# Kernel tuning notes

Measured on AMD Instinct MI355X. Metric: run time of the kernel, lower is better.

## Reference

```python
import jax, jax.numpy as jnp
import numpy as np

EPS = 1e-5

def _bn_train(h, gamma, beta):
    # BatchNorm1d in training mode: batch mean and biased variance over batch dim
    mu = jnp.mean(h, axis=0)
    var = jnp.mean((h - mu) ** 2, axis=0)
    return (h - mu) * jax.lax.rsqrt(var + EPS) * gamma + beta

def setup_inputs() -> dict:
    key = jax.random.key(0)
    ks = jax.random.split(key, 12)
    B, IN, H1, H2, NC = 16384, 4096, 256, 128, 12
    x = jax.random.normal(ks[0], (B, 1, 64, 64), dtype=jnp.float32)
    y = jax.random.randint(ks[1], (B,), 0, NC, dtype=jnp.int32)
    s1 = 1.0 / np.sqrt(IN)
    W1 = jax.random.uniform(ks[2], (H1, IN), jnp.float32, -s1, s1)
    b1 = jax.random.uniform(ks[3], (H1,), jnp.float32, -s1, s1)
    g1 = jax.random.normal(ks[4], (H1,), jnp.float32) * 0.1 + 1.0
    be1 = jax.random.normal(ks[5], (H1,), jnp.float32) * 0.1
    s2 = 1.0 / np.sqrt(H1)
    W2 = jax.random.uniform(ks[6], (H2, H1), jnp.float32, -s2, s2)
    b2 = jax.random.uniform(ks[7], (H2,), jnp.float32, -s2, s2)
    g2 = jax.random.normal(ks[8], (H2,), jnp.float32) * 0.1 + 1.0
    be2 = jax.random.normal(ks[9], (H2,), jnp.float32) * 0.1
    s4 = 1.0 / np.sqrt(H2)
    W4 = jax.random.uniform(ks[10], (NC, H2), jnp.float32, -s4, s4)
    b4 = jax.random.uniform(ks[11], (NC,), jnp.float32, -s4, s4)
    return {"x": x, "W1": W1, "b1": b1, "g1": g1, "be1": be1,
            "W2": W2, "b2": b2, "g2": g2, "be2": be2,
            "W4": W4, "b4": b4, "y": y}

def reference(x, W1, b1, g1, be1, W2, b2, g2, be2, W4, b4, y):
    B = x.shape[0]
    h = x.reshape(B, -1)  # [B, 4096]
    # layer 1: binarized linear + BN(train) + hardtanh (dropout p=0 is identity)
    h = h @ jnp.sign(W1).T + jnp.sign(b1)
    h = jnp.clip(_bn_train(h, g1, be1), -1.0, 1.0)
    # layer 2
    h = h @ jnp.sign(W2).T + jnp.sign(b2)
    h = jnp.clip(_bn_train(h, g2, be2), -1.0, 1.0)
    # final float linear
    return h @ W4.T + b4  # [B, 12]
```

## Files before the change

kernel.cpp:

```cpp
#include <hip/hip_runtime.h>
#include <cstddef>

typedef __attribute__((ext_vector_type(8))) short short8;
typedef __attribute__((ext_vector_type(4))) float f4;
typedef __attribute__((ext_vector_type(4))) unsigned int u4;

__device__ __forceinline__ unsigned int f2bf(float f){
  unsigned int u = __float_as_uint(f);
  u += 0x7fffu + ((u >> 16) & 1u);
  return u >> 16;
}
__device__ __forceinline__ float bflo(unsigned int w){ return __uint_as_float((w & 0xFFFFu) << 16); }
__device__ __forceinline__ float bfhi(unsigned int w){ return __uint_as_float(w & 0xFFFF0000u); }
__device__ __forceinline__ float fsign(float x){ return (x > 0.f) ? 1.f : ((x < 0.f) ? -1.f : 0.f); }
__device__ __forceinline__ float hclip(float x){ return fminf(1.f, fmaxf(-1.f, x)); }

#define BARRIER() do { \
    __builtin_amdgcn_sched_barrier(0); \
    asm volatile("s_waitcnt lgkmcnt(0)" ::: "memory"); \
    __builtin_amdgcn_s_barrier(); \
    asm volatile("" ::: "memory"); \
    __builtin_amdgcn_sched_barrier(0); \
  } while(0)

__global__ void prep_sign_k(const float* __restrict__ W1, unsigned short* __restrict__ w1s,
                            const float* __restrict__ W2, unsigned short* __restrict__ w2s){
  int i = (blockIdx.x * blockDim.x + threadIdx.x) * 8;
  const float* w; unsigned short* o; int off;
  if (i < 1048576){ w = W1; o = w1s; off = i; }
  else            { w = W2; o = w2s; off = i - 1048576; if (off >= 32768) return; }
  f4 a = *(const f4*)(w + off);
  f4 b = *(const f4*)(w + off + 4);
  unsigned short s[8];
  #pragma unroll
  for (int j = 0; j < 4; j++) s[j]   = (a[j] > 0.f) ? 0x3F80u : ((a[j] < 0.f) ? 0xBF80u : 0u);
  #pragma unroll
  for (int j = 0; j < 4; j++) s[4+j] = (b[j] > 0.f) ? 0x3F80u : ((b[j] < 0.f) ? 0xBF80u : 0u);
  u4 v;
  v.x = (unsigned)s[0] | ((unsigned)s[1] << 16);
  v.y = (unsigned)s[2] | ((unsigned)s[3] << 16);
  v.z = (unsigned)s[4] | ((unsigned)s[5] << 16);
  v.w = (unsigned)s[6] | ((unsigned)s[7] << 16);
  *(u4*)(o + off) = v;
}

__global__ __launch_bounds__(512) void gemm1_k(
    const float* __restrict__ x, const unsigned short* __restrict__ w1s,
    const float* __restrict__ b1, unsigned short* __restrict__ h1,
    float* __restrict__ part1s, float* __restrict__ part1q)
{
  __shared__ __align__(16) char lds[65536];
  const int tid  = threadIdx.x;
  const int lane = tid & 63;
  const int wid  = tid >> 6;
  const int cl   = lane & 15;
  const int g    = lane >> 4;
  const int klo  = g * 8;
  const int row0 = blockIdx.x * 64;

  const int am  = tid >> 3;
  const int ak0 = (tid & 7) * 8;
  const float* xA = x + (size_t)(row0 + am) * 4096 + ak0;
  const int aoff  = ((am * 128) + (ak0 * 2)) ^ ((am & 7) << 4);

  const unsigned short* wbase = w1s + (size_t)(wid * 32 + cl) * 4096 + klo;

  f4 acc[4][2];
  const f4 z = {0.f, 0.f, 0.f, 0.f};
  #pragma unroll
  for (int i = 0; i < 4; i++){ acc[i][0] = z; acc[i][1] = z; }

  f4 rA0a, rA0b, rA1a, rA1b, rA2a, rA2b, rA3a, rA3b;
  short8 Bq0, Bq1, Bq2, Bq3, Br0, Br1, Br2, Br3;

#define LOADA4(KB0) do { \
    rA0a = *(const f4*)(xA + (KB0+0)*64); rA0b = *(const f4*)(xA + (KB0+0)*64 + 4); \
    rA1a = *(const f4*)(xA + (KB0+1)*64); rA1b = *(const f4*)(xA + (KB0+1)*64 + 4); \
    rA2a = *(const f4*)(xA + (KB0+2)*64); rA2b = *(const f4*)(xA + (KB0+2)*64 + 4); \
    rA3a = *(const f4*)(xA + (KB0+3)*64); rA3b = *(const f4*)(xA + (KB0+3)*64 + 4); \
  } while(0)

#define PACK1(DST, RA, RB) do { \
    u4 _v; \
    _v.x = f2bf(RA[0]) | (f2bf(RA[1]) << 16); \
    _v.y = f2bf(RA[2]) | (f2bf(RA[3]) << 16); \
    _v.z = f2bf(RB[0]) | (f2bf(RB[1]) << 16); \
    _v.w = f2bf(RB[2]) | (f2bf(RB[3]) << 16); \
    *(u4*)(DST) = _v; \
  } while(0)

#define WRITEA4(WB) do { \
    PACK1((WB) +     0 + aoff, rA0a, rA0b); \
    PACK1((WB) +  8192 + aoff, rA1a, rA1b); \
    PACK1((WB) + 16384 + aoff, rA2a, rA2b); \
    PACK1((WB) + 24576 + aoff, rA3a, rA3b); \
  } while(0)

#define LOADB(P, KB) do { \
    B##P##0 = *(const short8*)(wbase + (KB)*64); \
    B##P##1 = *(const short8*)(wbase + (KB)*64 + 32); \
    B##P##2 = *(const short8*)(wbase + 65536 + (KB)*64); \
    B##P##3 = *(const short8*)(wbase + 65536 + (KB)*64 + 32); \
  } while(0)

#define COMPUTE(BASE, P) do { \
    const char* _ab = (const char*)(BASE); \
    short8 _af[4][2]; \
    _Pragma("unroll") \
    for (int fm = 0; fm < 4; fm++){ \
      int _m = fm*16 + cl; \
      _af[fm][0] = *(const short8*)(_ab + ((_m*128 + klo*2) ^ ((_m & 7) << 4))); \
      _af[fm][1] = *(const short8*)(_ab + ((_m*128 + (32 + klo)*2) ^ ((_m & 7) << 4))); \
    } \
    _Pragma("unroll") \
    for (int fm = 0; fm < 4; fm++){ \
      acc[fm][0] = __builtin_amdgcn_mfma_f32_16x16x32_bf16(_af[fm][0], B##P##0, acc[fm][0], 0, 0, 0); \
      acc[fm][1] = __builtin_amdgcn_mfma_f32_16x16x32_bf16(_af[fm][0], B##P##2, acc[fm][1], 0, 0, 0); \
      acc[fm][0] = __builtin_amdgcn_mfma_f32_16x16x32_bf16(_af[fm][1], B##P##1, acc[fm][0], 0, 0, 0); \
      acc[fm][1] = __builtin_amdgcn_mfma_f32_16x16x32_bf16(_af[fm][1], B##P##3, acc[fm][1], 0, 0, 0); \
    } \
  } while(0)

  LOADA4(0);
  WRITEA4(lds);
  LOADB(q, 0);
  BARRIER();

  for (int p = 0; p < 16; ++p){
    const bool pg = (p < 15);
    char* rbuf = lds + ((p & 1) << 15);
    char* wbuf = lds + (((p & 1) ^ 1) << 15);
    if (pg) LOADA4(4*p + 4);
    __builtin_amdgcn_sched_barrier(0);
    LOADB(r, 4*p + 1);
    COMPUTE(rbuf,         q);
    LOADB(q, 4*p + 2);
    COMPUTE(rbuf +  8192, r);
    LOADB(r, 4*p + 3);
    COMPUTE(rbuf + 16384, q);
    if (pg) LOADB(q, 4*p + 4);
    COMPUTE(rbuf + 24576, r);
    __builtin_amdgcn_sched_barrier(0);
    if (pg) WRITEA4(wbuf);
    BARRIER();
  }
#undef COMPUTE
#undef LOADB
#undef WRITEA4
#undef PACK1
#undef LOADA4

  #pragma unroll
  for (int fn = 0; fn < 2; fn++){
    int c = wid*32 + fn*16 + cl;
    float sb = fsign(b1[c]);
    float s = 0.f, q = 0.f;
    #pragma unroll
    for (int fm = 0; fm < 4; fm++){
      int rbase = row0 + fm*16 + g*4;
      #pragma unroll
      for (int i = 0; i < 4; i++){
        float v = acc[fm][fn][i] + sb;
        h1[(size_t)(rbase + i)*256 + c] = (unsigned short)f2bf(v);
        s += v; q += v*v;
      }
    }
    s += __shfl_xor(s, 16, 64); s += __shfl_xor(s, 32, 64);
    q += __shfl_xor(q, 16, 64); q += __shfl_xor(q, 32, 64);
    if (g == 0){
      part1s[c*256 + blockIdx.x] = s;
      part1q[c*256 + blockIdx.x] = q;
    }
  }
}

template<int COLS>
__global__ __launch_bounds__(64) void params_k(
    const float* __restrict__ ps, const float* __restrict__ pq,
    const float* __restrict__ g, const float* __restrict__ be,
    float* __restrict__ ab){
  int j = blockIdx.x * 64 + threadIdx.x;
  const f4* vs = (const f4*)(ps + j*256);
  const f4* vq = (const f4*)(pq + j*256);
  f4 s4 = {0,0,0,0}, q4 = {0,0,0,0};
  #pragma unroll 8
  for (int b = 0; b < 64; b++){ s4 += vs[b]; q4 += vq[b]; }
  float s = s4[0]+s4[1]+s4[2]+s4[3];
  float q = q4[0]+q4[1]+q4[2]+q4[3];
  float mu  = s * (1.f/16384.f);
  float var = q * (1.f/16384.f) - mu*mu;
  float a   = g[j] * rsqrtf(var + 1e-5f);
  ab[j] = a;
  ab[COLS + j] = be[j] - mu*a;
}

__global__ __launch_bounds__(512) void gemm2_k(
    const unsigned short* __restrict__ h1, const unsigned short* __restrict__ w2s,
    const float* __restrict__ b2, const float* __restrict__ ab1,
    unsigned short* __restrict__ h2, float* __restrict__ part2s, float* __restrict__ part2q)
{
  __shared__ __align__(16) char lds[32768];
  const int tid  = threadIdx.x;
  const int lane = tid & 63;
  const int wid  = tid >> 6;
  const int cl   = lane & 15;
  const int g    = lane >> 4;
  const int klo  = g * 8;
  const int row0 = blockIdx.x * 64;

  const int am  = tid >> 3;
  const int ak0 = (tid & 7) * 8;
  const unsigned short* hA = h1 + (size_t)(row0 + am) * 256 + ak0;
  const int aw = ((am * 128) + (ak0 * 2)) ^ ((am & 7) << 4);
  const unsigned short* wbase = w2s + (size_t)(wid * 16 + cl) * 256 + klo;

  u4 q0 = *(const u4*)(hA);
  u4 q1 = *(const u4*)(hA + 64);
  u4 q2 = *(const u4*)(hA + 128);
  u4 q3 = *(const u4*)(hA + 192);
  short8 Bq0, Bq1, Br0, Br1;
  Bq0 = *(const short8*)(wbase);
  Bq1 = *(const short8*)(wbase + 32);

#define TRW(KB, RAW) do { \
    f4 _a0 = *(const f4*)(ab1 + (KB)*64 + ak0); \
    f4 _a1 = *(const f4*)(ab1 + (KB)*64 + ak0 + 4); \
    f4 _c0 = *(const f4*)(ab1 + 256 + (KB)*64 + ak0); \
    f4 _c1 = *(const f4*)(ab1 + 256 + (KB)*64 + ak0 + 4); \
    float _t0 = hclip(_a0[0]*bflo(RAW.x) + _c0[0]); \
    float _t1 = hclip(_a0[1]*bfhi(RAW.x) + _c0[1]); \
    float _t2 = hclip(_a0[2]*bflo(RAW.y) + _c0[2]); \
    float _t3 = hclip(_a0[3]*bfhi(RAW.y) + _c0[3]); \
    float _t4 = hclip(_a1[0]*bflo(RAW.z) + _c1[0]); \
    float _t5 = hclip(_a1[1]*bfhi(RAW.z) + _c1[1]); \
    float _t6 = hclip(_a1[2]*bflo(RAW.w) + _c1[2]); \
    float _t7 = hclip(_a1[3]*bfhi(RAW.w) + _c1[3]); \
    u4 _v; \
    _v.x = f2bf(_t0) | (f2bf(_t1) << 16); \
    _v.y = f2bf(_t2) | (f2bf(_t3) << 16); \
    _v.z = f2bf(_t4) | (f2bf(_t5) << 16); \
    _v.w = f2bf(_t6) | (f2bf(_t7) << 16); \
    *(u4*)(lds + (KB)*8192 + aw) = _v; \
  } while(0)

  TRW(0, q0); TRW(1, q1); TRW(2, q2); TRW(3, q3);
#undef TRW
  BARRIER();

  f4 acc[4];
  const f4 z = {0.f, 0.f, 0.f, 0.f};
  #pragma unroll
  for (int i = 0; i < 4; i++) acc[i] = z;

#define LOADB2(P, KB) do { \
    B##P##0 = *(const short8*)(wbase + (KB)*64); \
    B##P##1 = *(const short8*)(wbase + (KB)*64 + 32); \
  } while(0)

#define COMP2(BASE, P) do { \
    const char* _ab = (const char*)(BASE); \
    short8 _af[4][2]; \
    _Pragma("unroll") \
    for (int fm = 0; fm < 4; fm++){ \
      int _m = fm*16 + cl; \
      _af[fm][0] = *(const short8*)(_ab + ((_m*128 + klo*2) ^ ((_m & 7) << 4))); \
      _af[fm][1] = *(const short8*)(_ab + ((_m*128 + (32 + klo)*2) ^ ((_m & 7) << 4))); \
    } \
    _Pragma("unroll") \
    for (int fm = 0; fm < 4; fm++){ \
      acc[fm] = __builtin_amdgcn_mfma_f32_16x16x32_bf16(_af[fm][0], B##P##0, acc[fm], 0, 0, 0); \
      acc[fm] = __builtin_amdgcn_mfma_f32_16x16x32_bf16(_af[fm][1], B##P##1, acc[fm], 0, 0, 0); \
    } \
  } while(0)

  LOADB2(r, 1);
  COMP2(lds,         q);
  LOADB2(q, 2);
  COMP2(lds +  8192, r);
  LOADB2(r, 3);
  COMP2(lds + 16384, q);
  COMP2(lds + 24576, r);
#undef COMP2
#undef LOADB2

  {
    int c = wid*16 + cl;
    float sb = fsign(b2[c]);
    float s = 0.f, q = 0.f;
    #pragma unroll
    for (int fm = 0; fm < 4; fm++){
      int rbase = row0 + fm*16 + g*4;
      #pragma unroll
      for (int i = 0; i < 4; i++){
        float v = acc[fm][i] + sb;
        h2[(size_t)(rbase + i)*128 + c] = (unsigned short)f2bf(v);
        s += v; q += v*v;
      }
    }
    s += __shfl_xor(s, 16, 64); s += __shfl_xor(s, 32, 64);
    q += __shfl_xor(q, 16, 64); q += __shfl_xor(q, 32, 64);
    if (g == 0){
      part2s[c*256 + blockIdx.x] = s;
      part2q[c*256 + blockIdx.x] = q;
    }
  }
}

__global__ __launch_bounds__(64) void final_k(
    const unsigned short* __restrict__ h2, const float* __restrict__ ab2,
    const float* __restrict__ W4, const float* __restrict__ b4,
    float* __restrict__ out)
{
  __shared__ __align__(16) float W4l[12*128];
  __shared__ __align__(16) float a2l[128];
  __shared__ __align__(16) float c2l[128];
  const int t = threadIdx.x;
  #pragma unroll
  for (int i = 0; i < 6; i++)
    *(f4*)&W4l[(i*64 + t)*4] = *(const f4*)(W4 + (i*64 + t)*4);
  a2l[t]      = ab2[t];
  a2l[t + 64] = ab2[t + 64];
  c2l[t]      = ab2[128 + t];
  c2l[t + 64] = ab2[192 + t];
  __syncthreads();

  const int r = blockIdx.x * 64 + t;
  const u4* hp = (const u4*)(h2 + (size_t)r * 128);
  u4 hv0 = hp[0], hv1 = hp[1], hv2 = hp[2],  hv3 = hp[3];
  u4 hv4 = hp[4], hv5 = hp[5], hv6 = hp[6],  hv7 = hp[7];
  u4 hv8 = hp[8], hv9 = hp[9], hv10 = hp[10], hv11 = hp[11];
  u4 hv12 = hp[12], hv13 = hp[13], hv14 = hp[14], hv15 = hp[15];

  float acc[12];
  #pragma unroll
  for (int o = 0; o < 12; o++) acc[o] = b4[o];

#define FPROC(HV, J) do { \
    f4 a0 = *(const f4*)&a2l[(J)*8];     f4 a1 = *(const f4*)&a2l[(J)*8 + 4]; \
    f4 c0 = *(const f4*)&c2l[(J)*8];     f4 c1 = *(const f4*)&c2l[(J)*8 + 4]; \
    float tt0 = hclip(a0[0]*bflo(HV.x) + c0[0]); \
    float tt1 = hclip(a0[1]*bfhi(HV.x) + c0[1]); \
    float tt2 = hclip(a0[2]*bflo(HV.y) + c0[2]); \
    float tt3 = hclip(a0[3]*bfhi(HV.y) + c0[3]); \
    float tt4 = hclip(a1[0]*bflo(HV.z) + c1[0]); \
    float tt5 = hclip(a1[1]*bfhi(HV.z) + c1[1]); \
    float tt6 = hclip(a1[2]*bflo(HV.w) + c1[2]); \
    float tt7 = hclip(a1[3]*bfhi(HV.w) + c1[3]); \
    _Pragma("unroll") \
    for (int o = 0; o < 12; o++){ \
      f4 w0 = *(const f4*)&W4l[o*128 + (J)*8]; \
      f4 w1 = *(const f4*)&W4l[o*128 + (J)*8 + 4]; \
      acc[o] += tt0*w0[0] + tt1*w0[1] + tt2*w0[2] + tt3*w0[3] \
              + tt4*w1[0] + tt5*w1[1] + tt6*w1[2] + tt7*w1[3]; \
    } \
  } while(0)

  FPROC(hv0, 0);  FPROC(hv1, 1);  FPROC(hv2, 2);   FPROC(hv3, 3);
  FPROC(hv4, 4);  FPROC(hv5, 5);  FPROC(hv6, 6);   FPROC(hv7, 7);
  FPROC(hv8, 8);  FPROC(hv9, 9);  FPROC(hv10, 10); FPROC(hv11, 11);
  FPROC(hv12, 12); FPROC(hv13, 13); FPROC(hv14, 14); FPROC(hv15, 15);
#undef FPROC

  #pragma unroll
  for (int o = 0; o < 12; o++) out[(size_t)r*12 + o] = acc[o];
}

extern "C" void kernel_launch(void* const* d_in, const int* in_sizes, int n_in,
                              void* d_out, int out_size, void* d_ws, size_t ws_size,
                              hipStream_t stream)
{
  const float* x   = (const float*)d_in[0];
  const float* W1  = (const float*)d_in[1];
  const float* b1  = (const float*)d_in[2];
  const float* g1  = (const float*)d_in[3];
  const float* be1 = (const float*)d_in[4];
  const float* W2  = (const float*)d_in[5];
  const float* b2  = (const float*)d_in[6];
  const float* g2  = (const float*)d_in[7];
  const float* be2 = (const float*)d_in[8];
  const float* W4  = (const float*)d_in[9];
  const float* b4  = (const float*)d_in[10];
  float* out = (float*)d_out;

  char* ws = (char*)d_ws;
  unsigned short* h1     = (unsigned short*)(ws);
  unsigned short* h2     = (unsigned short*)(ws + 8388608);
  unsigned short* w1s    = (unsigned short*)(ws + 12582912);
  unsigned short* w2s    = (unsigned short*)(ws + 14680064);
  float*          part1s = (float*)(ws + 14745600);
  float*          part1q = (float*)(ws + 15007744);
  float*          part2s = (float*)(ws + 15269888);
  float*          part2q = (float*)(ws + 15400960);
  float*          ab1    = (float*)(ws + 15532032);
  float*          ab2    = (float*)(ws + 15534080);

  prep_sign_k<<<528, 256, 0, stream>>>(W1, w1s, W2, w2s);
  gemm1_k<<<256, 512, 0, stream>>>(x, w1s, b1, h1, part1s, part1q);
  params_k<256><<<4, 64, 0, stream>>>(part1s, part1q, g1, be1, ab1);
  gemm2_k<<<256, 512, 0, stream>>>(h1, w2s, b2, ab1, h2, part2s, part2q);
  params_k<128><<<2, 64, 0, stream>>>(part2s, part2q, g2, be2, ab2);
  final_k<<<256, 64, 0, stream>>>(h2, ab2, W4, b4, out);
}
```

Baseline: 125.5 us.

## Retile gemm1 to 32-row blocks and fold BN param kernels into consumers

gemm1 now uses 256-thread blocks over 32 rows with 4 waves each covering 64 output columns. B fragments for two k-steps are loaded directly from global each iteration, and LDS use drops to 16KB. This doubles the grid to 512 blocks for better occupancy and CU coverage. The two params_k launches are removed: gemm2 reduces the layer-1 partials in every block, and final_k (now 128 threads) reduces the layer-2 partials. This saves launches at the cost of redundant per-block reductions.

```diff
diff --git a/kernel.cpp b/kernel.cpp
--- a/kernel.cpp
+++ b/kernel.cpp
@@ -44,40 +44,52 @@
   *(u4*)(o + off) = v;
 }
 
-__global__ __launch_bounds__(512) void gemm1_k(
+__global__ __launch_bounds__(256, 2) void gemm1_k(
     const float* __restrict__ x, const unsigned short* __restrict__ w1s,
     const float* __restrict__ b1, unsigned short* __restrict__ h1,
     float* __restrict__ part1s, float* __restrict__ part1q)
 {
-  __shared__ __align__(16) char lds[65536];
+  __shared__ __align__(16) char lds[16384];
   const int tid  = threadIdx.x;
   const int lane = tid & 63;
   const int wid  = tid >> 6;
   const int cl   = lane & 15;
   const int g    = lane >> 4;
   const int klo  = g * 8;
-  const int row0 = blockIdx.x * 64;
+  const int row0 = blockIdx.x * 32;
 
   const int am  = tid >> 3;
   const int ak0 = (tid & 7) * 8;
   const float* xA = x + (size_t)(row0 + am) * 4096 + ak0;
   const int aoff  = ((am * 128) + (ak0 * 2)) ^ ((am & 7) << 4);
 
-  const unsigned short* wbase = w1s + (size_t)(wid * 32 + cl) * 4096 + klo;
-
-  f4 acc[4][2];
+  const unsigned short* wbase = w1s + (size_t)(wid * 64 + cl) * 4096 + klo;
+
+  f4 acc[2][4];
   const f4 z = {0.f, 0.f, 0.f, 0.f};
   #pragma unroll
-  for (int i = 0; i < 4; i++){ acc[i][0] = z; acc[i][1] = z; }
-
-  f4 rA0a, rA0b, rA1a, rA1b, rA2a, rA2b, rA3a, rA3b;
-  short8 Bq0, Bq1, Bq2, Bq3, Br0, Br1, Br2, Br3;
-
-#define LOADA4(KB0) do { \
+  for (int i = 0; i < 2; i++)
+    #pragma unroll
+    for (int j = 0; j < 4; j++) acc[i][j] = z;
+
+  f4 rA0a, rA0b, rA1a, rA1b;
+  short8 BB0_0, BB0_1, BB0_2, BB0_3, BB0_4, BB0_5, BB0_6, BB0_7;
+  short8 BB1_0, BB1_1, BB1_2, BB1_3, BB1_4, BB1_5, BB1_6, BB1_7;
+
+#define LOADB8(S, KB) do { \
+    BB##S##_0 = *(const short8*)(wbase +          (KB)*64     ); \
+    BB##S##_1 = *(const short8*)(wbase +          (KB)*64 + 32); \
+    BB##S##_2 = *(const short8*)(wbase +  65536 + (KB)*64     ); \
+    BB##S##_3 = *(const short8*)(wbase +  65536 + (KB)*64 + 32); \
+    BB##S##_4 = *(const short8*)(wbase + 131072 + (KB)*64     ); \
+    BB##S##_5 = *(const short8*)(wbase + 131072 + (KB)*64 + 32); \
+    BB##S##_6 = *(const short8*)(wbase + 196608 + (KB)*64     ); \
+    BB##S##_7 = *(const short8*)(wbase + 196608 + (KB)*64 + 32); \
+  } while(0)
+
+#define LOADA2(KB0) do { \
     rA0a = *(const f4*)(xA + (KB0+0)*64); rA0b = *(const f4*)(xA + (KB0+0)*64 + 4); \
     rA1a = *(const f4*)(xA + (KB0+1)*64); rA1b = *(const f4*)(xA + (KB0+1)*64 + 4); \
-    rA2a = *(const f4*)(xA + (KB0+2)*64); rA2b = *(const f4*)(xA + (KB0+2)*64 + 4); \
-    rA3a = *(const f4*)(xA + (KB0+3)*64); rA3b = *(const f4*)(xA + (KB0+3)*64 + 4); \
   } while(0)
 
 #define PACK1(DST, RA, RB) do { \
@@ -89,74 +101,69 @@
     *(u4*)(DST) = _v; \
   } while(0)
 
-#define WRITEA4(WB) do { \
-    PACK1((WB) +     0 + aoff, rA0a, rA0b); \
-    PACK1((WB) +  8192 + aoff, rA1a, rA1b); \
-    PACK1((WB) + 16384 + aoff, rA2a, rA2b); \
-    PACK1((WB) + 24576 + aoff, rA3a, rA3b); \
-  } while(0)
-
-#define LOADB(P, KB) do { \
-    B##P##0 = *(const short8*)(wbase + (KB)*64); \
-    B##P##1 = *(const short8*)(wbase + (KB)*64 + 32); \
-    B##P##2 = *(const short8*)(wbase + 65536 + (KB)*64); \
-    B##P##3 = *(const short8*)(wbase + 65536 + (KB)*64 + 32); \
-  } while(0)
-
-#define COMPUTE(BASE, P) do { \
+#define WRITEA2(WB) do { \
+    PACK1((WB) +    0 + aoff, rA0a, rA0b); \
+    PACK1((WB) + 4096 + aoff, rA1a, rA1b); \
+  } while(0)
+
+#define COMPUTE1(BASE, S) do { \
     const char* _ab = (const char*)(BASE); \
-    short8 _af[4][2]; \
-    _Pragma("unroll") \
-    for (int fm = 0; fm < 4; fm++){ \
-      int _m = fm*16 + cl; \
-      _af[fm][0] = *(const short8*)(_ab + ((_m*128 + klo*2) ^ ((_m & 7) << 4))); \
-      _af[fm][1] = *(const short8*)(_ab + ((_m*128 + (32 + klo)*2) ^ ((_m & 7) << 4))); \
-    } \
-    _Pragma("unroll") \
-    for (int fm = 0; fm < 4; fm++){ \
-      acc[fm][0] = __builtin_amdgcn_mfma_f32_16x16x32_bf16(_af[fm][0], B##P##0, acc[fm][0], 0, 0, 0); \
-      acc[fm][1] = __builtin_amdgcn_mfma_f32_16x16x32_bf16(_af[fm][0], B##P##2, acc[fm][1], 0, 0, 0); \
-      acc[fm][0] = __builtin_amdgcn_mfma_f32_16x16x32_bf16(_af[fm][1], B##P##1, acc[fm][0], 0, 0, 0); \
-      acc[fm][1] = __builtin_amdgcn_mfma_f32_16x16x32_bf16(_af[fm][1], B##P##3, acc[fm][1], 0, 0, 0); \
-    } \
-  } while(0)
-
-  LOADA4(0);
-  WRITEA4(lds);
-  LOADB(q, 0);
+    short8 _a0k0, _a0k1, _a1k0, _a1k1; \
+    { int _m = cl; \
+      _a0k0 = *(const short8*)(_ab + ((_m*128 +      klo*2) ^ ((_m & 7) << 4))); \
+      _a0k1 = *(const short8*)(_ab + ((_m*128 + 64 + klo*2) ^ ((_m & 7) << 4))); } \
+    { int _m = 16 + cl; \
+      _a1k0 = *(const short8*)(_ab + ((_m*128 +      klo*2) ^ ((_m & 7) << 4))); \
+      _a1k1 = *(const short8*)(_ab + ((_m*128 + 64 + klo*2) ^ ((_m & 7) << 4))); } \
+    acc[0][0] = __builtin_amdgcn_mfma_f32_16x16x32_bf16(_a0k0, BB##S##_0, acc[0][0], 0, 0, 0); \
+    acc[0][1] = __builtin_amdgcn_mfma_f32_16x16x32_bf16(_a0k0, BB##S##_2, acc[0][1], 0, 0, 0); \
+    acc[0][2] = __builtin_amdgcn_mfma_f32_16x16x32_bf16(_a0k0, BB##S##_4, acc[0][2], 0, 0, 0); \
+    acc[0][3] = __builtin_amdgcn_mfma_f32_16x16x32_bf16(_a0k0, BB##S##_6, acc[0][3], 0, 0, 0); \
+    acc[1][0] = __builtin_amdgcn_mfma_f32_16x16x32_bf16(_a1k0, BB##S##_0, acc[1][0], 0, 0, 0); \
+    acc[1][1] = __builtin_amdgcn_mfma_f32_16x16x32_bf16(_a1k0, BB##S##_2, acc[1][1], 0, 0, 0); \
+    acc[1][2] = __builtin_amdgcn_mfma_f32_16x16x32_bf16(_a1k0, BB##S##_4, acc[1][2], 0, 0, 0); \
+    acc[1][3] = __builtin_amdgcn_mfma_f32_16x16x32_bf16(_a1k0, BB##S##_6, acc[1][3], 0, 0, 0); \
+    acc[0][0] = __builtin_amdgcn_mfma_f32_16x16x32_bf16(_a0k1, BB##S##_1, acc[0][0], 0, 0, 0); \
+    acc[0][1] = __builtin_amdgcn_mfma_f32_16x16x32_bf16(_a0k1, BB##S##_3, acc[0][1], 0, 0, 0); \
+    acc[0][2] = __builtin_amdgcn_mfma_f32_16x16x32_bf16(_a0k1, BB##S##_5, acc[0][2], 0, 0, 0); \
+    acc[0][3] = __builtin_amdgcn_mfma_f32_16x16x32_bf16(_a0k1, BB##S##_7, acc[0][3], 0, 0, 0); \
+    acc[1][0] = __builtin_amdgcn_mfma_f32_16x16x32_bf16(_a1k1, BB##S##_1, acc[1][0], 0, 0, 0); \
+    acc[1][1] = __builtin_amdgcn_mfma_f32_16x16x32_bf16(_a1k1, BB##S##_3, acc[1][1], 0, 0, 0); \
+    acc[1][2] = __builtin_amdgcn_mfma_f32_16x16x32_bf16(_a1k1, BB##S##_5, acc[1][2], 0, 0, 0); \
+    acc[1][3] = __builtin_amdgcn_mfma_f32_16x16x32_bf16(_a1k1, BB##S##_7, acc[1][3], 0, 0, 0); \
+  } while(0)
+
+  LOADA2(0);
+  WRITEA2(lds);
   BARRIER();
 
-  for (int p = 0; p < 16; ++p){
-    const bool pg = (p < 15);
-    char* rbuf = lds + ((p & 1) << 15);
-    char* wbuf = lds + (((p & 1) ^ 1) << 15);
-    if (pg) LOADA4(4*p + 4);
+  for (int p = 0; p < 32; ++p){
+    char* rb = lds + ((p & 1) << 13);
+    char* wb = lds + (((p & 1) ^ 1) << 13);
+    LOADB8(0, 2*p);
+    LOADB8(1, 2*p + 1);
     __builtin_amdgcn_sched_barrier(0);
-    LOADB(r, 4*p + 1);
-    COMPUTE(rbuf,         q);
-    LOADB(q, 4*p + 2);
-    COMPUTE(rbuf +  8192, r);
-    LOADB(r, 4*p + 3);
-    COMPUTE(rbuf + 16384, q);
-    if (pg) LOADB(q, 4*p + 4);
-    COMPUTE(rbuf + 24576, r);
+    if (p < 31) LOADA2(2*p + 2);
     __builtin_amdgcn_sched_barrier(0);
-    if (pg) WRITEA4(wbuf);
+    COMPUTE1(rb,        0);
+    COMPUTE1(rb + 4096, 1);
+    __builtin_amdgcn_sched_barrier(0);
+    if (p < 31) WRITEA2(wb);
     BARRIER();
   }
-#undef COMPUTE
-#undef LOADB
-#undef WRITEA4
+#undef COMPUTE1
+#undef WRITEA2
 #undef PACK1
-#undef LOADA4
-
-  #pragma unroll
-  for (int fn = 0; fn < 2; fn++){
-    int c = wid*32 + fn*16 + cl;
+#undef LOADA2
+#undef LOADB8
+
+  #pragma unroll
+  for (int fn = 0; fn < 4; fn++){
+    int c = wid*64 + fn*16 + cl;
     float sb = fsign(b1[c]);
     float s = 0.f, q = 0.f;
     #pragma unroll
-    for (int fm = 0; fm < 4; fm++){
+    for (int fm = 0; fm < 2; fm++){
       int rbase = row0 + fm*16 + g*4;
       #pragma unroll
       for (int i = 0; i < 4; i++){
@@ -168,38 +175,24 @@
     s += __shfl_xor(s, 16, 64); s += __shfl_xor(s, 32, 64);
     q += __shfl_xor(q, 16, 64); q += __shfl_xor(q, 32, 64);
     if (g == 0){
-      part1s[c*256 + blockIdx.x] = s;
-      part1q[c*256 + blockIdx.x] = q;
+      part1s[c*512 + blockIdx.x] = s;
+      part1q[c*512 + blockIdx.x] = q;
     }
   }
-}
-
-template<int COLS>
-__global__ __launch_bounds__(64) void params_k(
-    const float* __restrict__ ps, const float* __restrict__ pq,
-    const float* __restrict__ g, const float* __restrict__ be,
-    float* __restrict__ ab){
-  int j = blockIdx.x * 64 + threadIdx.x;
-  const f4* vs = (const f4*)(ps + j*256);
-  const f4* vq = (const f4*)(pq + j*256);
-  f4 s4 = {0,0,0,0}, q4 = {0,0,0,0};
-  #pragma unroll 8
-  for (int b = 0; b < 64; b++){ s4 += vs[b]; q4 += vq[b]; }
-  float s = s4[0]+s4[1]+s4[2]+s4[3];
-  float q = q4[0]+q4[1]+q4[2]+q4[3];
-  float mu  = s * (1.f/16384.f);
-  float var = q * (1.f/16384.f) - mu*mu;
-  float a   = g[j] * rsqrtf(var + 1e-5f);
-  ab[j] = a;
-  ab[COLS + j] = be[j] - mu*a;
 }
 
 __global__ __launch_bounds__(512) void gemm2_k(
     const unsigned short* __restrict__ h1, const unsigned short* __restrict__ w2s,
-    const float* __restrict__ b2, const float* __restrict__ ab1,
+    const float* __restrict__ b2,
+    const float* __restrict__ part1s, const float* __restrict__ part1q,
+    const float* __restrict__ g1, const float* __restrict__ be1,
     unsigned short* __restrict__ h2, float* __restrict__ part2s, float* __restrict__ part2q)
 {
   __shared__ __align__(16) char lds[32768];
+  __shared__ __align__(16) float a1l[256];
+  __shared__ __align__(16) float c1l[256];
+  __shared__ __align__(16) float sred[512];
+  __shared__ __align__(16) float qred[512];
   const int tid  = threadIdx.x;
   const int lane = tid & 63;
   const int wid  = tid >> 6;
@@ -222,11 +215,33 @@
   Bq0 = *(const short8*)(wbase);
   Bq1 = *(const short8*)(wbase + 32);
 
+  {
+    const int col = tid & 255, half = tid >> 8;
+    const f4* vs = (const f4*)(part1s + col*512 + half*256);
+    const f4* vq = (const f4*)(part1q + col*512 + half*256);
+    f4 s4 = {0,0,0,0}, q4 = {0,0,0,0};
+    #pragma unroll 8
+    for (int b = 0; b < 64; b++){ s4 += vs[b]; q4 += vq[b]; }
+    sred[tid] = s4[0]+s4[1]+s4[2]+s4[3];
+    qred[tid] = q4[0]+q4[1]+q4[2]+q4[3];
+  }
+  BARRIER();
+  if (tid < 256){
+    float s = sred[tid] + sred[256 + tid];
+    float q = qred[tid] + qred[256 + tid];
+    float mu  = s * (1.f/16384.f);
+    float var = q * (1.f/16384.f) - mu*mu;
+    float a   = g1[tid] * rsqrtf(var + 1e-5f);
+    a1l[tid] = a;
+    c1l[tid] = be1[tid] - mu*a;
+  }
+  BARRIER();
+
 #define TRW(KB, RAW) do { \
-    f4 _a0 = *(const f4*)(ab1 + (KB)*64 + ak0); \
-    f4 _a1 = *(const f4*)(ab1 + (KB)*64 + ak0 + 4); \
-    f4 _c0 = *(const f4*)(ab1 + 256 + (KB)*64 + ak0); \
-    f4 _c1 = *(const f4*)(ab1 + 256 + (KB)*64 + ak0 + 4); \
+    f4 _a0 = *(const f4*)(&a1l[(KB)*64 + ak0]); \
+    f4 _a1 = *(const f4*)(&a1l[(KB)*64 + ak0 + 4]); \
+    f4 _c0 = *(const f4*)(&c1l[(KB)*64 + ak0]); \
+    f4 _c1 = *(const f4*)(&c1l[(KB)*64 + ak0 + 4]); \
     float _t0 = hclip(_a0[0]*bflo(RAW.x) + _c0[0]); \
     float _t1 = hclip(_a0[1]*bfhi(RAW.x) + _c0[1]); \
     float _t2 = hclip(_a0[2]*bflo(RAW.y) + _c0[2]); \
@@ -306,8 +321,10 @@
   }
 }
 
-__global__ __launch_bounds__(64) void final_k(
-    const unsigned short* __restrict__ h2, const float* __restrict__ ab2,
+__global__ __launch_bounds__(128) void final_k(
+    const unsigned short* __restrict__ h2,
+    const float* __restrict__ part2s, const float* __restrict__ part2q,
+    const float* __restrict__ g2, const float* __restrict__ be2,
     const float* __restrict__ W4, const float* __restrict__ b4,
     float* __restrict__ out)
 {
@@ -316,15 +333,25 @@
   __shared__ __align__(16) float c2l[128];
   const int t = threadIdx.x;
   #pragma unroll
-  for (int i = 0; i < 6; i++)
-    *(f4*)&W4l[(i*64 + t)*4] = *(const f4*)(W4 + (i*64 + t)*4);
-  a2l[t]      = ab2[t];
-  a2l[t + 64] = ab2[t + 64];
-  c2l[t]      = ab2[128 + t];
-  c2l[t + 64] = ab2[192 + t];
+  for (int i = 0; i < 3; i++)
+    *(f4*)&W4l[(i*128 + t)*4] = *(const f4*)(W4 + (i*128 + t)*4);
+  {
+    const f4* vs = (const f4*)(part2s + t*256);
+    const f4* vq = (const f4*)(part2q + t*256);
+    f4 s4 = {0,0,0,0}, q4 = {0,0,0,0};
+    #pragma unroll 8
+    for (int b = 0; b < 64; b++){ s4 += vs[b]; q4 += vq[b]; }
+    float s = s4[0]+s4[1]+s4[2]+s4[3];
+    float q = q4[0]+q4[1]+q4[2]+q4[3];
+    float mu  = s * (1.f/16384.f);
+    float var = q * (1.f/16384.f) - mu*mu;
+    float a   = g2[t] * rsqrtf(var + 1e-5f);
+    a2l[t] = a;
+    c2l[t] = be2[t] - mu*a;
+  }
   __syncthreads();
 
-  const int r = blockIdx.x * 64 + t;
+  const int r = blockIdx.x * 128 + t;
   const u4* hp = (const u4*)(h2 + (size_t)r * 128);
   u4 hv0 = hp[0], hv1 = hp[1], hv2 = hp[2],  hv3 = hp[3];
   u4 hv4 = hp[4], hv5 = hp[5], hv6 = hp[6],  hv7 = hp[7];
@@ -388,16 +415,12 @@
   unsigned short* w1s    = (unsigned short*)(ws + 12582912);
   unsigned short* w2s    = (unsigned short*)(ws + 14680064);
   float*          part1s = (float*)(ws + 14745600);
-  float*          part1q = (float*)(ws + 15007744);
-  float*          part2s = (float*)(ws + 15269888);
-  float*          part2q = (float*)(ws + 15400960);
-  float*          ab1    = (float*)(ws + 15532032);
-  float*          ab2    = (float*)(ws + 15534080);
+  float*          part1q = (float*)(ws + 15269888);
+  float*          part2s = (float*)(ws + 15794176);
+  float*          part2q = (float*)(ws + 15925248);
 
   prep_sign_k<<<528, 256, 0, stream>>>(W1, w1s, W2, w2s);
-  gemm1_k<<<256, 512, 0, stream>>>(x, w1s, b1, h1, part1s, part1q);
-  params_k<256><<<4, 64, 0, stream>>>(part1s, part1q, g1, be1, ab1);
-  gemm2_k<<<256, 512, 0, stream>>>(h1, w2s, b2, ab1, h2, part2s, part2q);
-  params_k<128><<<2, 64, 0, stream>>>(part2s, part2q, g2, be2, ab2);
-  final_k<<<256, 64, 0, stream>>>(h2, ab2, W4, b4, out);
-}
+  gemm1_k<<<512, 256, 0, stream>>>(x, w1s, b1, h1, part1s, part1q);
+  gemm2_k<<<256, 512, 0, stream>>>(h1, w2s, b2, part1s, part1q, g1, be1, h2, part2s, part2q);
+  final_k<<<128, 128, 0, stream>>>(h2, part2s, part2q, g2, be2, W4, b4, out);
+}
```

Measured after the change: 199.8 us. 59.3% more time.
